# Kernel optimization log

Hardware: AMD Instinct MI355X
Metric: run time of the kernel (lower is better)

The kernel has to match this reference:

```python
import jax, jax.numpy as jnp
import numpy as np

SIGMA1 = 0.02   # sigma1 init arg
K = 128         # number of discretization bins
TMIN = 1e-10
LEAKY_SLOPE = 0.01  # torch nn.LeakyReLU default


def setup_inputs() -> dict:
    key = jax.random.key(0)
    k1, k2, k3, k4, k5 = jax.random.split(key, 5)
    B, D, H = 256, 1024, 2048
    x = jax.random.uniform(k1, (B, D), jnp.float32, -1.0, 1.0)
    t = jax.random.uniform(k2, (B, 1), jnp.float32)          # Uniform(0,1) time sample
    noise = jax.random.normal(k3, (B, D), jnp.float32)       # for Normal sample of mu
    W1 = jax.random.normal(k4, (D + 1, H), jnp.float32) * (1.0 / np.sqrt(D + 1))
    b1 = jnp.zeros((H,), jnp.float32)
    W2 = jax.random.normal(k5, (H, 2 * D), jnp.float32) * (1.0 / np.sqrt(H))
    b2 = jnp.zeros((2 * D,), jnp.float32)
    return dict(x=x, t=t, noise=noise, W1=W1, b1=b1, W2=W2, b2=b2)


def _discretised_output_distribution(mu, t, gamma, W1, b1, W2, b2):
    B, D = mu.shape
    # NN: Linear -> LeakyReLU -> Linear, split into mu_eps / ln_sigma_eps
    h = jnp.concatenate([mu, t], axis=1) @ W1 + b1
    h = jnp.where(h >= 0, h, LEAKY_SLOPE * h)
    out = h @ W2 + b2
    mu_eps, ln_sig_eps = out[:, :D], out[:, D:]

    r = jnp.sqrt((1.0 - gamma) / gamma)                      # (B,1)
    mu_x = mu / gamma - r * mu_eps                           # (B,D)
    sigma_x = r * jnp.exp(ln_sig_eps)                        # (B,D)

    low_t = t < TMIN                                         # (B,1) rows with tiny t
    mu_x = jnp.where(low_t, 0.0, mu_x)
    sigma_x = jnp.where(low_t, 1.0, sigma_x)

    k = jnp.arange(K, dtype=jnp.float32)
    kl = 2.0 * (k - 1.0) / K - 1.0                           # left bin edge
    kr = 2.0 * k / K - 1.0                                   # right bin edge
    kc = (2.0 * k - 1.0) / K - 1.0                           # bin center weight

    inv = 1.0 / (sigma_x * jnp.sqrt(jnp.float32(2.0)))       # (B,D)

    def cdf(bound):  # bound: (K,) scalars -> clamped discretized CDF (B,D,K)
        F = 0.5 * (1.0 + jax.lax.erf((bound[None, None, :] - mu_x[:, :, None]) * inv[:, :, None]))
        return jnp.where(bound <= -1.0, 0.0, jnp.where(bound >= 1.0, 1.0, F))

    p = kc * (cdf(kr) - cdf(kl))                             # (B,D,K)
    return jnp.sum(p, axis=-1)                               # (B,D) expected value


def reference(x, t, noise, W1, b1, W2, b2):
    gamma = 1.0 - SIGMA1 ** (2.0 * t)                        # (B,1)
    # mu ~ Normal(gamma*x, std=gamma*(1-gamma)), reparameterized with noise
    mu = gamma * x + gamma * (1.0 - gamma) * noise
    pO = _discretised_output_distribution(mu, t, gamma, W1, b1, W2, b2)
    se = (x - pO) ** 2                                       # elementwise MSE
    loss = -jnp.log(jnp.float32(SIGMA1)) * jnp.mean(SIGMA1 ** (-2.0 * t) * se)
    return loss
```

## Files before the change

kernel.cpp:

```cpp
#include <hip/hip_runtime.h>
#include <hip/hip_bf16.h>
#include <math.h>


typedef __bf16 bf16_t;
typedef __bf16 bf16x8 __attribute__((ext_vector_type(8)));
typedef __bf16 bf16x4 __attribute__((ext_vector_type(4)));
typedef float  f32x4  __attribute__((ext_vector_type(4)));

#define LDK 40
#define L2S -5.6438561897747248f

__device__ __forceinline__ float erf_f(float x) {
  float ax = __builtin_fabsf(x);
  float t = __builtin_amdgcn_rcpf(fmaf(0.3275911f, ax, 1.0f));
  float p = fmaf(fmaf(fmaf(fmaf(1.061405429f, t, -1.453152027f), t, 1.421413741f),
                      t, -0.284496736f), t, 0.254829592f);
  p *= t;
  float e = __expf(-ax * ax);
  float r = fmaf(-p, e, 1.0f);
  return __builtin_copysignf(r, x);
}

__global__ __launch_bounds__(256, 2)
void prep_k(const float* __restrict__ x, const float* __restrict__ noise,
            const float* __restrict__ t, bf16_t* __restrict__ A1) {
  int b = blockIdx.x;
  float tv = t[b];
  float p = exp2f(2.0f * tv * L2S);
  float g = 1.0f - p, gom = g * p;
  int e = (b * 256 + threadIdx.x) * 4;
  float4 xv = *(const float4*)(x + e);
  float4 nv = *(const float4*)(noise + e);
  bf16x4 o;
  o[0] = (__bf16)fmaf(gom, nv.x, g * xv.x);
  o[1] = (__bf16)fmaf(gom, nv.y, g * xv.y);
  o[2] = (__bf16)fmaf(gom, nv.z, g * xv.z);
  o[3] = (__bf16)fmaf(gom, nv.w, g * xv.w);
  *(bf16x4*)(A1 + e) = o;
}

__global__ __launch_bounds__(256, 2)
void gemm_k(const bf16_t* __restrict__ A, int lda,
            const float* __restrict__ W, int N,
            float* __restrict__ P, int Ktiles, int Kchunk) {
  __shared__ bf16_t As[256 * LDK];
  __shared__ bf16_t Bs[32 * LDK];
  int tid = threadIdx.x;
  int lane = tid & 63, wave = tid >> 6;
  int n0 = blockIdx.x * 32;
  int k0 = blockIdx.z * Kchunk;
  int bn = tid & 31, bkg = tid >> 5;
  int fm = lane & 15, kq = lane >> 4;

  f32x4 acc[4][2];
#pragma unroll
  for (int i = 0; i < 4; ++i)
#pragma unroll
    for (int j = 0; j < 2; ++j) acc[i][j] = (f32x4)0.0f;

  for (int kt = 0; kt < Ktiles; ++kt) {
    int kb = k0 + kt * 32;
    const bf16_t* Ar = A + (size_t)tid * lda + kb;
#pragma unroll
    for (int j = 0; j < 4; ++j)
      *(bf16x8*)(&As[tid * LDK + j * 8]) = *(const bf16x8*)(Ar + j * 8);
    {
      const float* Wp = W + (size_t)(kb + bkg * 4) * N + n0 + bn;
      bf16x4 bv;
#pragma unroll
      for (int i = 0; i < 4; ++i) bv[i] = (__bf16)Wp[(size_t)i * N];
      *(bf16x4*)(&Bs[bn * LDK + bkg * 4]) = bv;
    }
    __syncthreads();
    bf16x8 aF[4], bF[2];
#pragma unroll
    for (int i = 0; i < 4; ++i)
      aF[i] = *(const bf16x8*)(&As[(wave * 64 + i * 16 + fm) * LDK + kq * 8]);
#pragma unroll
    for (int j = 0; j < 2; ++j)
      bF[j] = *(const bf16x8*)(&Bs[(j * 16 + fm) * LDK + kq * 8]);
#pragma unroll
    for (int i = 0; i < 4; ++i)
#pragma unroll
      for (int j = 0; j < 2; ++j)
        acc[i][j] = __builtin_amdgcn_mfma_f32_16x16x32_bf16(aF[i], bF[j], acc[i][j], 0, 0, 0);
    __syncthreads();
  }
  float* Pp = P + (size_t)blockIdx.z * 256 * N + n0;
#pragma unroll
  for (int i = 0; i < 4; ++i) {
    int mrow = wave * 64 + i * 16 + kq * 4;
#pragma unroll
    for (int j = 0; j < 2; ++j)
#pragma unroll
      for (int r = 0; r < 4; ++r)
        Pp[(size_t)(mrow + r) * N + j * 16 + fm] = acc[i][j][r];
  }
}

__global__ __launch_bounds__(256, 2)
void reduce1_k(const float* __restrict__ P1, const float* __restrict__ W1,
               const float* __restrict__ b1, const float* __restrict__ t,
               bf16_t* __restrict__ h, float* __restrict__ out) {
  if (blockIdx.x == 0 && threadIdx.x == 0) *out = 0.0f;
  int e = (blockIdx.x * 256 + threadIdx.x) * 4;
  int b = e >> 11, n = e & 2047;
  float4 s = *(const float4*)(P1 + e);
#pragma unroll
  for (int sp = 1; sp < 8; ++sp) {
    float4 v = *(const float4*)(P1 + (size_t)sp * 524288 + e);
    s.x += v.x; s.y += v.y; s.z += v.z; s.w += v.w;
  }
  float tv = t[b];
  float4 wl = *(const float4*)(W1 + 1024 * 2048 + n);
  float4 bb = *(const float4*)(b1 + n);
  s.x += tv * wl.x + bb.x;
  s.y += tv * wl.y + bb.y;
  s.z += tv * wl.z + bb.z;
  s.w += tv * wl.w + bb.w;
  bf16x4 o;
  o[0] = (__bf16)(s.x >= 0.f ? s.x : 0.01f * s.x);
  o[1] = (__bf16)(s.y >= 0.f ? s.y : 0.01f * s.y);
  o[2] = (__bf16)(s.z >= 0.f ? s.z : 0.01f * s.z);
  o[3] = (__bf16)(s.w >= 0.f ? s.w : 0.01f * s.w);
  *(bf16x4*)(h + e) = o;
}

__global__ __launch_bounds__(256, 4)
void loss_k(const float* __restrict__ x, const float* __restrict__ noise,
            const float* __restrict__ P2, const float* __restrict__ b2,
            const float* __restrict__ t, float* __restrict__ out) {
  int gid = blockIdx.x * 256 + threadIdx.x;
  int b = gid >> 10, d = gid & 1023;
  float tv = t[b];
  float om = exp2f(2.0f * tv * L2S);
  float gamma = 1.0f - om;
  float r = sqrtf(om / gamma);
  float w = 1.0f / om;
  bool lowt = tv < 1e-10f;
  int base2 = b * 2048 + d;
  float me = b2[d], lg = b2[1024 + d];
#pragma unroll
  for (int sp = 0; sp < 8; ++sp) {
    me += P2[(size_t)sp * 524288 + base2];
    lg += P2[(size_t)sp * 524288 + base2 + 1024];
  }
  float xs = x[gid], ns = noise[gid];

  float mu_x = xs + om * ns - r * me;
  float sig = r * __expf(lg);
  if (lowt) { mu_x = 0.f; sig = 1.f; }
  float invs = 0.70710678118654752f / sig;
  float a = invs * 0.015625f;
  float c0 = (1.f + mu_x) * invs;
  float m64 = 64.f * (1.f + mu_x);
  float wdt = 316.78383797157331f * sig;
  float lo = m64 - wdt, hi = m64 + wdt;
  int klo = (lo < 1.f) ? 1 : ((lo > 126.f) ? 127 : (int)ceilf(lo));
  int khi = (hi < 1.f) ? 0 : ((hi > 126.f) ? 126 : (int)floorf(hi));
  float ss = (float)(126 - khi) - (float)(klo - 1);
  if (khi >= klo) {
    if (a <= 1.0f) {
      float za = fmaf(a, (float)klo - 0.5f, -c0);
      float zb = fmaf(a, (float)khi + 0.5f, -c0);
      const float ISP = 0.56418958354775628f;
      float ea = __expf(-za * za), eb = __expf(-zb * zb);
      float Ga = fmaf(za, erf_f(za), ISP * ea);
      float Gb = fmaf(zb, erf_f(zb), ISP * eb);
      float S = (Gb - Ga) * __builtin_amdgcn_rcpf(a)
              - a * 0.047015889f * (eb - ea);
      ss += S;
    } else {
      for (int k = klo; k <= khi; ++k) ss += erf_f(fmaf(a, (float)k, -c0));
    }
  }
  float z127 = fmaf(a, 127.f, -c0);
  float pO = fmaf(0.48828125f, 1.f + erf_f(z127),
                  fmaf(-0.0078125f, ss, -0.984375f));
  float df = xs - pO;
  float accv = w * df * df;
#pragma unroll
  for (int off = 32; off > 0; off >>= 1) accv += __shfl_down(accv, off, 64);
  __shared__ float red[4];
  if ((threadIdx.x & 63) == 0) red[threadIdx.x >> 6] = accv;
  __syncthreads();
  if (threadIdx.x == 0) {
    const float SCALE = 3.9120230054281461f / 262144.0f;
    atomicAdd(out, (red[0] + red[1] + red[2] + red[3]) * SCALE);
  }
}

extern "C" void kernel_launch(void* const* d_in, const int* in_sizes, int n_in,
                              void* d_out, int out_size, void* d_ws, size_t ws_size,
                              hipStream_t stream) {
  const float* x     = (const float*)d_in[0];
  const float* t     = (const float*)d_in[1];
  const float* noise = (const float*)d_in[2];
  const float* W1    = (const float*)d_in[3];
  const float* b1    = (const float*)d_in[4];
  const float* W2    = (const float*)d_in[5];
  const float* b2    = (const float*)d_in[6];
  float* out = (float*)d_out;

  char* ws = (char*)d_ws;
  bf16_t* A1 = (bf16_t*)ws;
  bf16_t* h  = (bf16_t*)(ws + 524288);
  float*  P1 = (float*)(ws + 524288 + 1048576);
  float*  P2 = (float*)(ws + 524288 + 1048576 + 16777216);

  prep_k<<<256, 256, 0, stream>>>(x, noise, t, A1);
  gemm_k<<<dim3(64, 1, 8), 256, 0, stream>>>(A1, 1024, W1, 2048, P1, 4, 128);
  reduce1_k<<<512, 256, 0, stream>>>(P1, W1, b1, t, h, out);
  gemm_k<<<dim3(64, 1, 8), 256, 0, stream>>>(h, 2048, W2, 2048, P2, 8, 256);
  loss_k<<<1024, 256, 0, stream>>>(x, noise, P2, b2, t, out);
}
```

Baseline: 123.1 us.

## Double-buffer GEMM shared tiles and prefetch next K-tile into registers

The GEMM kernel now keeps two LDS buffers and register-prefetches the next A/W tile from global memory while the current tile is consumed by MFMAs. One of the two barriers per iteration is dropped and replaced by an explicit lgkmcnt wait plus raw s_barrier. The goal is to hide global load latency behind compute. Costs are more registers and LDS, and the single barrier with ping-pong buffers must still keep writes to a buffer from overlapping reads of the same buffer two iterations earlier.

```diff
diff --git a/kernel.cpp b/kernel.cpp
--- a/kernel.cpp
+++ b/kernel.cpp
@@ -44,8 +44,8 @@
 void gemm_k(const bf16_t* __restrict__ A, int lda,
             const float* __restrict__ W, int N,
             float* __restrict__ P, int Ktiles, int Kchunk) {
-  __shared__ bf16_t As[256 * LDK];
-  __shared__ bf16_t Bs[32 * LDK];
+  __shared__ bf16_t As[2][256 * LDK];
+  __shared__ bf16_t Bs[2][32 * LDK];
   int tid = threadIdx.x;
   int lane = tid & 63, wave = tid >> 6;
   int n0 = blockIdx.x * 32;
@@ -53,39 +53,59 @@
   int bn = tid & 31, bkg = tid >> 5;
   int fm = lane & 15, kq = lane >> 4;
 
+  const bf16_t* Arow = A + (size_t)tid * lda + k0;
+  const float*  Wcol = W + (size_t)(k0 + bkg * 4) * N + n0 + bn;
+
   f32x4 acc[4][2];
 #pragma unroll
   for (int i = 0; i < 4; ++i)
 #pragma unroll
     for (int j = 0; j < 2; ++j) acc[i][j] = (f32x4)0.0f;
 
+  bf16x8 aR[4];
+  float  bR[4];
+#pragma unroll
+  for (int j = 0; j < 4; ++j) aR[j] = *(const bf16x8*)(Arow + j * 8);
+#pragma unroll
+  for (int i = 0; i < 4; ++i) bR[i] = Wcol[(size_t)i * N];
+
   for (int kt = 0; kt < Ktiles; ++kt) {
-    int kb = k0 + kt * 32;
-    const bf16_t* Ar = A + (size_t)tid * lda + kb;
+    int cur = kt & 1;
+    bf16_t* as = &As[cur][0];
+    bf16_t* bs = &Bs[cur][0];
 #pragma unroll
     for (int j = 0; j < 4; ++j)
-      *(bf16x8*)(&As[tid * LDK + j * 8]) = *(const bf16x8*)(Ar + j * 8);
+      *(bf16x8*)(&as[tid * LDK + j * 8]) = aR[j];
     {
-      const float* Wp = W + (size_t)(kb + bkg * 4) * N + n0 + bn;
       bf16x4 bv;
 #pragma unroll
-      for (int i = 0; i < 4; ++i) bv[i] = (__bf16)Wp[(size_t)i * N];
-      *(bf16x4*)(&Bs[bn * LDK + bkg * 4]) = bv;
+      for (int i = 0; i < 4; ++i) bv[i] = (__bf16)bR[i];
+      *(bf16x4*)(&bs[bn * LDK + bkg * 4]) = bv;
     }
-    __syncthreads();
+    if (kt + 1 < Ktiles) {
+      const bf16_t* Ar = Arow + (kt + 1) * 32;
+#pragma unroll
+      for (int j = 0; j < 4; ++j) aR[j] = *(const bf16x8*)(Ar + j * 8);
+      const float* Wp = Wcol + (size_t)(kt + 1) * 32 * N;
+#pragma unroll
+      for (int i = 0; i < 4; ++i) bR[i] = Wp[(size_t)i * N];
+    }
+    asm volatile("s_waitcnt lgkmcnt(0)" ::: "memory");
+    __builtin_amdgcn_s_barrier();
+    __builtin_amdgcn_sched_barrier(0);
+
     bf16x8 aF[4], bF[2];
 #pragma unroll
     for (int i = 0; i < 4; ++i)
-      aF[i] = *(const bf16x8*)(&As[(wave * 64 + i * 16 + fm) * LDK + kq * 8]);
+      aF[i] = *(const bf16x8*)(&as[(wave * 64 + i * 16 + fm) * LDK + kq * 8]);
 #pragma unroll
     for (int j = 0; j < 2; ++j)
-      bF[j] = *(const bf16x8*)(&Bs[(j * 16 + fm) * LDK + kq * 8]);
+      bF[j] = *(const bf16x8*)(&bs[(j * 16 + fm) * LDK + kq * 8]);
 #pragma unroll
     for (int i = 0; i < 4; ++i)
 #pragma unroll
       for (int j = 0; j < 2; ++j)
         acc[i][j] = __builtin_amdgcn_mfma_f32_16x16x32_bf16(aF[i], bF[j], acc[i][j], 0, 0, 0);
-    __syncthreads();
   }
   float* Pp = P + (size_t)blockIdx.z * 256 * N + n0;
 #pragma unroll
```

Measured after the change: 123.1 us. Within noise of the previous version (-0.0%).

## Replace split-K GEMMs with M-tiled GEMMs fused with bias/activation and loss epilogues

Applied to the files above, without the earlier changes.

Drops the split-K partial-sum buffers and the separate reduce and loss kernels. Each GEMM now tiles over M (64 rows per block) and runs the full K loop, with bias, LeakyReLU and bf16 store fused into the first GEMM's epilogue and the whole discretized-loss computation fused into the second. The K loop gains register prefetch four tiles ahead and LDS double buffering with a single barrier per step. This removes about 32 MB of fp32 partial traffic and two launches, but each block now walks a much longer serial K loop and has less MFMA work per tile, so per-block latency goes up.

```diff
diff --git a/kernel.cpp b/kernel.cpp
--- a/kernel.cpp
+++ b/kernel.cpp
@@ -24,7 +24,9 @@
 
 __global__ __launch_bounds__(256, 2)
 void prep_k(const float* __restrict__ x, const float* __restrict__ noise,
-            const float* __restrict__ t, bf16_t* __restrict__ A1) {
+            const float* __restrict__ t, bf16_t* __restrict__ A1,
+            float* __restrict__ out) {
+  if (blockIdx.x == 0 && threadIdx.x == 0) *out = 0.0f;
   int b = blockIdx.x;
   float tv = t[b];
   float p = exp2f(2.0f * tv * L2S);
@@ -40,152 +42,173 @@
   *(bf16x4*)(A1 + e) = o;
 }
 
+#define GSTEP(ASB, BSB, AR, BR, TILE, PF)                                        \
+  {                                                                              \
+    *(bf16x8*)(&ASB[arow * LDK + akg * 8]) = AR;                                 \
+    bf16x4 bv_;                                                                  \
+    bv_[0] = (__bf16)BR[0]; bv_[1] = (__bf16)BR[1];                              \
+    bv_[2] = (__bf16)BR[2]; bv_[3] = (__bf16)BR[3];                              \
+    *(bf16x4*)(&BSB[bn * LDK + bkg * 4]) = bv_;                                  \
+    if (PF) {                                                                    \
+      AR = *(const bf16x8*)(Ap + ((TILE) + 4) * 32);                             \
+      const float* wp_ = Wp0 + (size_t)((TILE) + 4) * 32 * 2048;                 \
+      BR[0] = wp_[0]; BR[1] = wp_[2048]; BR[2] = wp_[4096]; BR[3] = wp_[6144];   \
+    }                                                                            \
+    asm volatile("s_waitcnt lgkmcnt(0)" ::: "memory");                           \
+    __builtin_amdgcn_s_barrier();                                                \
+    __builtin_amdgcn_sched_barrier(0);                                           \
+    {                                                                            \
+      bf16x8 aF_ = *(const bf16x8*)(&ASB[(wave * 16 + fm) * LDK + kq * 8]);      \
+      bf16x8 bF0_ = *(const bf16x8*)(&BSB[fm * LDK + kq * 8]);                   \
+      bf16x8 bF1_ = *(const bf16x8*)(&BSB[(16 + fm) * LDK + kq * 8]);            \
+      acc0 = __builtin_amdgcn_mfma_f32_16x16x32_bf16(aF_, bF0_, acc0, 0, 0, 0);  \
+      acc1 = __builtin_amdgcn_mfma_f32_16x16x32_bf16(aF_, bF1_, acc1, 0, 0, 0);  \
+    }                                                                            \
+  }
+
+__device__ __forceinline__ void gemm_loop(
+    const bf16_t* __restrict__ Ap, const float* __restrict__ Wp0,
+    bf16_t* __restrict__ As0, bf16_t* __restrict__ As1,
+    bf16_t* __restrict__ Bs0, bf16_t* __restrict__ Bs1,
+    int arow, int akg, int bn, int bkg, int wave, int fm, int kq,
+    int Ktiles, f32x4& acc0, f32x4& acc1) {
+  bf16x8 aR0, aR1, aR2, aR3;
+  f32x4 bR0, bR1, bR2, bR3;
+  aR0 = *(const bf16x8*)(Ap);
+  aR1 = *(const bf16x8*)(Ap + 32);
+  aR2 = *(const bf16x8*)(Ap + 64);
+  aR3 = *(const bf16x8*)(Ap + 96);
+  {
+    const float* w_ = Wp0;
+    bR0[0] = w_[0]; bR0[1] = w_[2048]; bR0[2] = w_[4096]; bR0[3] = w_[6144];
+    w_ = Wp0 + (size_t)32 * 2048;
+    bR1[0] = w_[0]; bR1[1] = w_[2048]; bR1[2] = w_[4096]; bR1[3] = w_[6144];
+    w_ = Wp0 + (size_t)64 * 2048;
+    bR2[0] = w_[0]; bR2[1] = w_[2048]; bR2[2] = w_[4096]; bR2[3] = w_[6144];
+    w_ = Wp0 + (size_t)96 * 2048;
+    bR3[0] = w_[0]; bR3[1] = w_[2048]; bR3[2] = w_[4096]; bR3[3] = w_[6144];
+  }
+  for (int kt = 0; kt < Ktiles; kt += 4) {
+    GSTEP(As0, Bs0, aR0, bR0, kt,     kt + 4 < Ktiles)
+    GSTEP(As1, Bs1, aR1, bR1, kt + 1, kt + 5 < Ktiles)
+    GSTEP(As0, Bs0, aR2, bR2, kt + 2, kt + 6 < Ktiles)
+    GSTEP(As1, Bs1, aR3, bR3, kt + 3, kt + 7 < Ktiles)
+  }
+}
+
 __global__ __launch_bounds__(256, 2)
-void gemm_k(const bf16_t* __restrict__ A, int lda,
-            const float* __restrict__ W, int N,
-            float* __restrict__ P, int Ktiles, int Kchunk) {
-  __shared__ bf16_t As[256 * LDK];
-  __shared__ bf16_t Bs[32 * LDK];
+void gemm1h_k(const bf16_t* __restrict__ A, const float* __restrict__ W,
+              const float* __restrict__ b1, const float* __restrict__ t,
+              bf16_t* __restrict__ h) {
+  __shared__ bf16_t As0[64 * LDK], As1[64 * LDK];
+  __shared__ bf16_t Bs0[32 * LDK], Bs1[32 * LDK];
   int tid = threadIdx.x;
   int lane = tid & 63, wave = tid >> 6;
-  int n0 = blockIdx.x * 32;
-  int k0 = blockIdx.z * Kchunk;
+  int n0 = blockIdx.x * 32, m0 = blockIdx.y * 64;
+  int arow = tid >> 2, akg = tid & 3;
   int bn = tid & 31, bkg = tid >> 5;
   int fm = lane & 15, kq = lane >> 4;
 
-  f32x4 acc[4][2];
+  const bf16_t* Ap = A + (size_t)(m0 + arow) * 1024 + akg * 8;
+  const float* Wp0 = W + (size_t)(bkg * 4) * 2048 + n0 + bn;
+
+  f32x4 acc0 = (f32x4)0.0f, acc1 = (f32x4)0.0f;
+  gemm_loop(Ap, Wp0, As0, As1, Bs0, Bs1, arow, akg, bn, bkg, wave, fm, kq,
+            32, acc0, acc1);
+
+  int col0 = n0 + fm, col1 = n0 + 16 + fm;
+  float wl0 = W[(size_t)1024 * 2048 + col0], wl1 = W[(size_t)1024 * 2048 + col1];
+  float bb0 = b1[col0], bb1 = b1[col1];
 #pragma unroll
-  for (int i = 0; i < 4; ++i)
+  for (int e = 0; e < 4; ++e) {
+    int row = m0 + wave * 16 + kq * 4 + e;
+    float tv = t[row];
+    float v0 = acc0[e] + tv * wl0 + bb0;
+    float v1 = acc1[e] + tv * wl1 + bb1;
+    v0 = v0 >= 0.f ? v0 : 0.01f * v0;
+    v1 = v1 >= 0.f ? v1 : 0.01f * v1;
+    h[(size_t)row * 2048 + col0] = (__bf16)v0;
+    h[(size_t)row * 2048 + col1] = (__bf16)v1;
+  }
+}
+
+__global__ __launch_bounds__(256, 2)
+void gemm2loss_k(const bf16_t* __restrict__ A, const float* __restrict__ W,
+                 const float* __restrict__ b2, const float* __restrict__ t,
+                 const float* __restrict__ x, const float* __restrict__ noise,
+                 float* __restrict__ out) {
+  __shared__ bf16_t As0[64 * LDK], As1[64 * LDK];
+  __shared__ bf16_t Bs0[32 * LDK], Bs1[32 * LDK];
+  __shared__ float red[4];
+  int tid = threadIdx.x;
+  int lane = tid & 63, wave = tid >> 6;
+  int n0 = blockIdx.x * 16, m0 = blockIdx.y * 64;
+  int arow = tid >> 2, akg = tid & 3;
+  int bn = tid & 31, bkg = tid >> 5;
+  int fm = lane & 15, kq = lane >> 4;
+
+  const bf16_t* Ap = A + (size_t)(m0 + arow) * 2048 + akg * 8;
+  int bcol = n0 + (bn & 15) + ((bn >> 4) << 10);
+  const float* Wp0 = W + (size_t)(bkg * 4) * 2048 + bcol;
+
+  f32x4 acc0 = (f32x4)0.0f, acc1 = (f32x4)0.0f;
+  gemm_loop(Ap, Wp0, As0, As1, Bs0, Bs1, arow, akg, bn, bkg, wave, fm, kq,
+            64, acc0, acc1);
+
+  int d = n0 + fm;
+  float bme = b2[d], blg = b2[1024 + d];
+  float lsum = 0.0f;
 #pragma unroll
-    for (int j = 0; j < 2; ++j) acc[i][j] = (f32x4)0.0f;
-
-  for (int kt = 0; kt < Ktiles; ++kt) {
-    int kb = k0 + kt * 32;
-    const bf16_t* Ar = A + (size_t)tid * lda + kb;
+  for (int e = 0; e < 4; ++e) {
+    int row = m0 + wave * 16 + kq * 4 + e;
+    float tv = t[row];
+    float om = exp2f(2.0f * tv * L2S);
+    float gamma = 1.0f - om;
+    float rq = sqrtf(om / gamma);
+    float w = 1.0f / om;
+    bool lowt = tv < 1e-10f;
+    float me = acc0[e] + bme;
+    float lg = acc1[e] + blg;
+    float xs = x[(size_t)row * 1024 + d], ns = noise[(size_t)row * 1024 + d];
+
+    float mu_x = xs + om * ns - rq * me;
+    float sig = rq * __expf(lg);
+    if (lowt) { mu_x = 0.f; sig = 1.f; }
+    float invs = 0.70710678118654752f / sig;
+    float a = invs * 0.015625f;
+    float c0 = (1.f + mu_x) * invs;
+    float m64 = 64.f * (1.f + mu_x);
+    float wdt = 316.78383797157331f * sig;
+    float lo = m64 - wdt, hi = m64 + wdt;
+    int klo = (lo < 1.f) ? 1 : ((lo > 126.f) ? 127 : (int)ceilf(lo));
+    int khi = (hi < 1.f) ? 0 : ((hi > 126.f) ? 126 : (int)floorf(hi));
+    float ss = (float)(126 - khi) - (float)(klo - 1);
+    if (khi >= klo) {
+      if (a <= 1.0f) {
+        float za = fmaf(a, (float)klo - 0.5f, -c0);
+        float zb = fmaf(a, (float)khi + 0.5f, -c0);
+        const float ISP = 0.56418958354775628f;
+        float ea = __expf(-za * za), eb = __expf(-zb * zb);
+        float Ga = fmaf(za, erf_f(za), ISP * ea);
+        float Gb = fmaf(zb, erf_f(zb), ISP * eb);
+        float S = (Gb - Ga) * __builtin_amdgcn_rcpf(a)
+                - a * 0.047015889f * (eb - ea);
+        ss += S;
+      } else {
+        for (int k = klo; k <= khi; ++k) ss += erf_f(fmaf(a, (float)k, -c0));
+      }
+    }
+    float z127 = fmaf(a, 127.f, -c0);
+    float pO = fmaf(0.48828125f, 1.f + erf_f(z127),
+                    fmaf(-0.0078125f, ss, -0.984375f));
+    float df = xs - pO;
+    lsum += w * df * df;
+  }
 #pragma unroll
-    for (int j = 0; j < 4; ++j)
-      *(bf16x8*)(&As[tid * LDK + j * 8]) = *(const bf16x8*)(Ar + j * 8);
-    {
-      const float* Wp = W + (size_t)(kb + bkg * 4) * N + n0 + bn;
-      bf16x4 bv;
-#pragma unroll
-      for (int i = 0; i < 4; ++i) bv[i] = (__bf16)Wp[(size_t)i * N];
-      *(bf16x4*)(&Bs[bn * LDK + bkg * 4]) = bv;
-    }
-    __syncthreads();
-    bf16x8 aF[4], bF[2];
-#pragma unroll
-    for (int i = 0; i < 4; ++i)
-      aF[i] = *(const bf16x8*)(&As[(wave * 64 + i * 16 + fm) * LDK + kq * 8]);
-#pragma unroll
-    for (int j = 0; j < 2; ++j)
-      bF[j] = *(const bf16x8*)(&Bs[(j * 16 + fm) * LDK + kq * 8]);
-#pragma unroll
-    for (int i = 0; i < 4; ++i)
-#pragma unroll
-      for (int j = 0; j < 2; ++j)
-        acc[i][j] = __builtin_amdgcn_mfma_f32_16x16x32_bf16(aF[i], bF[j], acc[i][j], 0, 0, 0);
-    __syncthreads();
-  }
-  float* Pp = P + (size_t)blockIdx.z * 256 * N + n0;
-#pragma unroll
-  for (int i = 0; i < 4; ++i) {
-    int mrow = wave * 64 + i * 16 + kq * 4;
-#pragma unroll
-    for (int j = 0; j < 2; ++j)
-#pragma unroll
-      for (int r = 0; r < 4; ++r)
-        Pp[(size_t)(mrow + r) * N + j * 16 + fm] = acc[i][j][r];
-  }
-}
-
-__global__ __launch_bounds__(256, 2)
-void reduce1_k(const float* __restrict__ P1, const float* __restrict__ W1,
-               const float* __restrict__ b1, const float* __restrict__ t,
-               bf16_t* __restrict__ h, float* __restrict__ out) {
-  if (blockIdx.x == 0 && threadIdx.x == 0) *out = 0.0f;
-  int e = (blockIdx.x * 256 + threadIdx.x) * 4;
-  int b = e >> 11, n = e & 2047;
-  float4 s = *(const float4*)(P1 + e);
-#pragma unroll
-  for (int sp = 1; sp < 8; ++sp) {
-    float4 v = *(const float4*)(P1 + (size_t)sp * 524288 + e);
-    s.x += v.x; s.y += v.y; s.z += v.z; s.w += v.w;
-  }
-  float tv = t[b];
-  float4 wl = *(const float4*)(W1 + 1024 * 2048 + n);
-  float4 bb = *(const float4*)(b1 + n);
-  s.x += tv * wl.x + bb.x;
-  s.y += tv * wl.y + bb.y;
-  s.z += tv * wl.z + bb.z;
-  s.w += tv * wl.w + bb.w;
-  bf16x4 o;
-  o[0] = (__bf16)(s.x >= 0.f ? s.x : 0.01f * s.x);
-  o[1] = (__bf16)(s.y >= 0.f ? s.y : 0.01f * s.y);
-  o[2] = (__bf16)(s.z >= 0.f ? s.z : 0.01f * s.z);
-  o[3] = (__bf16)(s.w >= 0.f ? s.w : 0.01f * s.w);
-  *(bf16x4*)(h + e) = o;
-}
-
-__global__ __launch_bounds__(256, 4)
-void loss_k(const float* __restrict__ x, const float* __restrict__ noise,
-            const float* __restrict__ P2, const float* __restrict__ b2,
-            const float* __restrict__ t, float* __restrict__ out) {
-  int gid = blockIdx.x * 256 + threadIdx.x;
-  int b = gid >> 10, d = gid & 1023;
-  float tv = t[b];
-  float om = exp2f(2.0f * tv * L2S);
-  float gamma = 1.0f - om;
-  float r = sqrtf(om / gamma);
-  float w = 1.0f / om;
-  bool lowt = tv < 1e-10f;
-  int base2 = b * 2048 + d;
-  float me = b2[d], lg = b2[1024 + d];
-#pragma unroll
-  for (int sp = 0; sp < 8; ++sp) {
-    me += P2[(size_t)sp * 524288 + base2];
-    lg += P2[(size_t)sp * 524288 + base2 + 1024];
-  }
-  float xs = x[gid], ns = noise[gid];
-
-  float mu_x = xs + om * ns - r * me;
-  float sig = r * __expf(lg);
-  if (lowt) { mu_x = 0.f; sig = 1.f; }
-  float invs = 0.70710678118654752f / sig;
-  float a = invs * 0.015625f;
-  float c0 = (1.f + mu_x) * invs;
-  float m64 = 64.f * (1.f + mu_x);
-  float wdt = 316.78383797157331f * sig;
-  float lo = m64 - wdt, hi = m64 + wdt;
-  int klo = (lo < 1.f) ? 1 : ((lo > 126.f) ? 127 : (int)ceilf(lo));
-  int khi = (hi < 1.f) ? 0 : ((hi > 126.f) ? 126 : (int)floorf(hi));
-  float ss = (float)(126 - khi) - (float)(klo - 1);
-  if (khi >= klo) {
-    if (a <= 1.0f) {
-      float za = fmaf(a, (float)klo - 0.5f, -c0);
-      float zb = fmaf(a, (float)khi + 0.5f, -c0);
-      const float ISP = 0.56418958354775628f;
-      float ea = __expf(-za * za), eb = __expf(-zb * zb);
-      float Ga = fmaf(za, erf_f(za), ISP * ea);
-      float Gb = fmaf(zb, erf_f(zb), ISP * eb);
-      float S = (Gb - Ga) * __builtin_amdgcn_rcpf(a)
-              - a * 0.047015889f * (eb - ea);
-      ss += S;
-    } else {
-      for (int k = klo; k <= khi; ++k) ss += erf_f(fmaf(a, (float)k, -c0));
-    }
-  }
-  float z127 = fmaf(a, 127.f, -c0);
-  float pO = fmaf(0.48828125f, 1.f + erf_f(z127),
-                  fmaf(-0.0078125f, ss, -0.984375f));
-  float df = xs - pO;
-  float accv = w * df * df;
-#pragma unroll
-  for (int off = 32; off > 0; off >>= 1) accv += __shfl_down(accv, off, 64);
-  __shared__ float red[4];
-  if ((threadIdx.x & 63) == 0) red[threadIdx.x >> 6] = accv;
+  for (int off = 32; off > 0; off >>= 1) lsum += __shfl_down(lsum, off, 64);
+  if ((tid & 63) == 0) red[wave] = lsum;
   __syncthreads();
-  if (threadIdx.x == 0) {
+  if (tid == 0) {
     const float SCALE = 3.9120230054281461f / 262144.0f;
     atomicAdd(out, (red[0] + red[1] + red[2] + red[3]) * SCALE);
   }
@@ -206,12 +229,8 @@
   char* ws = (char*)d_ws;
   bf16_t* A1 = (bf16_t*)ws;
   bf16_t* h  = (bf16_t*)(ws + 524288);
-  float*  P1 = (float*)(ws + 524288 + 1048576);
-  float*  P2 = (float*)(ws + 524288 + 1048576 + 16777216);
-
-  prep_k<<<256, 256, 0, stream>>>(x, noise, t, A1);
-  gemm_k<<<dim3(64, 1, 8), 256, 0, stream>>>(A1, 1024, W1, 2048, P1, 4, 128);
-  reduce1_k<<<512, 256, 0, stream>>>(P1, W1, b1, t, h, out);
-  gemm_k<<<dim3(64, 1, 8), 256, 0, stream>>>(h, 2048, W2, 2048, P2, 8, 256);
-  loss_k<<<1024, 256, 0, stream>>>(x, noise, P2, b2, t, out);
-}
+
+  prep_k<<<256, 256, 0, stream>>>(x, noise, t, A1, out);
+  gemm1h_k<<<dim3(64, 4), 256, 0, stream>>>(A1, W1, b1, t, h);
+  gemm2loss_k<<<dim3(64, 4), 256, 0, stream>>>(h, W2, b2, t, x, noise, out);
+}
```

New measurement: 112.4 us. 1.1x faster.
